# Performance work log

Measured on AMD Instinct MI355X. Metric: run time of the kernel, lower is better.

Reference implementation:

```python
import jax, jax.numpy as jnp
import numpy as np

B, S, D, H, FF = 4, 2048, 1024, 16, 4096
HD = D // H


def setup_inputs() -> dict:
    key = jax.random.key(0)
    ks = jax.random.split(key, 12)
    s = 1.0 / np.sqrt(D)
    sf = 1.0 / np.sqrt(FF)
    return {
        "x": jax.random.normal(ks[0], (B, S, D), dtype=jnp.float32),
        "lengths": jax.random.randint(ks[1], (B,), 1, S + 1, dtype=jnp.int32),
        "qW": jax.random.uniform(ks[2], (D, D), jnp.float32, -s, s),
        "qb": jnp.zeros((D,), jnp.float32),
        "kW": jax.random.uniform(ks[3], (D, D), jnp.float32, -s, s),
        "kb": jnp.zeros((D,), jnp.float32),
        "vW": jax.random.uniform(ks[4], (D, D), jnp.float32, -s, s),
        "vb": jnp.zeros((D,), jnp.float32),
        "oW": jax.random.uniform(ks[5], (D, D), jnp.float32, -s, s),
        "ob": jnp.zeros((D,), jnp.float32),
        "w1": jax.random.uniform(ks[6], (D, FF), jnp.float32, -s, s),
        "b1": jnp.zeros((FF,), jnp.float32),
        "w2": jax.random.uniform(ks[7], (FF, D), jnp.float32, -sf, sf),
        "b2": jnp.zeros((D,), jnp.float32),
    }


def _heads(t):
    # [B,S,D] -> [B,H,S,HD]
    return t.reshape(B, S, H, HD).transpose(0, 2, 1, 3)


def reference(x, lengths, qW, qb, kW, kb, vW, vb, oW, ob, w1, b1, w2, b2):
    q = _heads(x @ qW + qb)
    k = _heads(x @ kW + kb)
    v = _heads(x @ vW + vb)
    scale = 1.0 / np.sqrt(HD)
    logits = jnp.einsum("bhqd,bhkd->bhqk", q, k) * scale  # [B,H,S,S]
    # key-position mask: pos >= length -> -inf
    mask = jnp.arange(S)[None, None, None, :] >= lengths[:, None, None, None]
    logits = jnp.where(mask, -jnp.inf, logits)
    a = jax.nn.softmax(logits, axis=-1)
    ctx = jnp.einsum("bhqk,bhkd->bhqd", a, v)
    ctx = ctx.transpose(0, 2, 1, 3).reshape(B, S, D)
    attn_out = ctx @ oW + ob
    h = jax.nn.relu(attn_out @ w1 + b1)
    return h @ w2 + b2
```

## Files before the change

kernel.cpp:

```cpp
#include <hip/hip_runtime.h>


typedef short bf16x8 __attribute__((ext_vector_type(8)));
typedef float f32x4 __attribute__((ext_vector_type(4)));

__device__ __forceinline__ unsigned short f2bf(float f) {
  unsigned int u = __builtin_bit_cast(unsigned int, f);
  u += 0x7fffu + ((u >> 16) & 1u);
  return (unsigned short)(u >> 16);
}

__device__ __forceinline__ void gload16(const unsigned short* g, unsigned short* l) {
  __builtin_amdgcn_global_load_lds(
      (const __attribute__((address_space(1))) unsigned int*)(g),
      (__attribute__((address_space(3))) unsigned int*)(l),
      16, 0, 0);
}

__global__ __launch_bounds__(256) void cast_f32_bf16(
    const float* __restrict__ src, unsigned short* __restrict__ dst, int n4) {
  int i = blockIdx.x * 256 + threadIdx.x;
  if (i < n4) {
    float4 f = ((const float4*)src)[i];
    ushort4 o;
    o.x = f2bf(f.x); o.y = f2bf(f.y); o.z = f2bf(f.z); o.w = f2bf(f.w);
    ((ushort4*)dst)[i] = o;
  }
}

__global__ __launch_bounds__(256) void prep_weights(
    const float* __restrict__ qW, const float* __restrict__ kW,
    const float* __restrict__ vW, const float* __restrict__ oW,
    const float* __restrict__ w1, const float* __restrict__ w2,
    unsigned short* __restrict__ qWt, unsigned short* __restrict__ kWt,
    unsigned short* __restrict__ vWt, unsigned short* __restrict__ oWt,
    unsigned short* __restrict__ w1t, unsigned short* __restrict__ w2t) {
  const int t = blockIdx.x;
  const float* W; unsigned short* Wt; int N, K, nt, kt;
  if (t < 2048) {
    const int w = t >> 9, r = t & 511;
    nt = r & 15; kt = r >> 4; N = 1024; K = 1024;
    W  = w == 0 ? qW : w == 1 ? kW : w == 2 ? vW : oW;
    Wt = w == 0 ? qWt : w == 1 ? kWt : w == 2 ? vWt : oWt;
  } else if (t < 4096) {
    const int r = t - 2048;
    nt = r & 63; kt = r >> 6; N = 4096; K = 1024; W = w1; Wt = w1t;
  } else {
    const int r = t - 4096;
    nt = r & 15; kt = r >> 4; N = 1024; K = 4096; W = w2; Wt = w2t;
  }
  const int wave = threadIdx.x >> 6, lane = threadIdx.x & 63;
  const int n = nt * 64 + lane;
  const int k0 = kt * 32 + wave * 8;
  union { int4 v; unsigned short u[8]; } s;
#pragma unroll
  for (int j = 0; j < 8; ++j) s.u[j] = f2bf(W[(size_t)(k0 + j) * N + n]);
  *(int4*)(Wt + (size_t)n * K + k0) = s.v;
}

__device__ __forceinline__ void gemm256_core(
    const unsigned short* __restrict__ A, const unsigned short* __restrict__ Bt,
    unsigned short* __restrict__ As, unsigned short* __restrict__ Bs,
    const int m0, const int n0, const int K, f32x4 (&acc)[8][4]) {
  const int tid = (int)threadIdx.x;
  const int w = tid >> 6, l = tid & 63;
  const int quad = l >> 4, l16 = l & 15;
  const int wm = (w >> 2) * 128, wn = (w & 3) * 64;

  const int lr = l >> 2, lc = l & 3;
  const int swz = (lc ^ ((l >> 3) & 3)) * 8;
  const unsigned short* gA[2]; const unsigned short* gB[2];
  unsigned short* dA[2]; unsigned short* dB[2];
#pragma unroll
  for (int j = 0; j < 2; ++j) {
    const int rr = (w * 2 + j) * 16 + lr;
    gA[j] = A + (size_t)(m0 + rr) * K + swz;
    gB[j] = Bt + (size_t)(n0 + rr) * K + swz;
    dA[j] = As + (w * 2 + j) * 512;
    dB[j] = Bs + (w * 2 + j) * 512;
  }

  const int cread = (quad ^ ((l16 >> 1) & 3)) * 8;
  const int rA = (wm + l16) * 32;
  const int rB = (wn + l16) * 32;

  auto STAGE = [&](int db, int t) {
#pragma unroll
    for (int j = 0; j < 2; ++j) {
      gload16(gA[j] + t * 32, dA[j] + db * 8192);
      gload16(gB[j] + t * 32, dB[j] + db * 8192);
    }
  };
  auto COMPUTE = [&](int db) {
    bf16x8 af[8], bf[4];
    const unsigned short* pa = As + db * 8192 + rA + cread;
    const unsigned short* pb = Bs + db * 8192 + rB + cread;
#pragma unroll
    for (int ni = 0; ni < 4; ++ni) bf[ni] = *(const bf16x8*)(pb + ni * 16 * 32);
#pragma unroll
    for (int mi = 0; mi < 8; ++mi) af[mi] = *(const bf16x8*)(pa + mi * 16 * 32);
    __builtin_amdgcn_s_setprio(1);
#pragma unroll
    for (int mi = 0; mi < 8; ++mi)
#pragma unroll
      for (int ni = 0; ni < 4; ++ni)
        acc[mi][ni] = __builtin_amdgcn_mfma_f32_16x16x32_bf16(
            af[mi], bf[ni], acc[mi][ni], 0, 0, 0);
    __builtin_amdgcn_s_setprio(0);
  };

  const int NK = K >> 5;
  STAGE(0, 0); STAGE(1, 1); STAGE(2, 2);
#pragma unroll 1
  for (int t = 0; t < NK - 3; ++t) {
    asm volatile("s_waitcnt vmcnt(8)" ::: "memory");
    __builtin_amdgcn_s_barrier();
    STAGE((t + 3) & 3, t + 3);
    COMPUTE(t & 3);
  }
  asm volatile("s_waitcnt vmcnt(8)" ::: "memory");
  __builtin_amdgcn_s_barrier();
  COMPUTE((NK - 3) & 3);
  asm volatile("s_waitcnt vmcnt(4)" ::: "memory");
  __builtin_amdgcn_s_barrier();
  COMPUTE((NK - 2) & 3);
  asm volatile("s_waitcnt vmcnt(0)" ::: "memory");
  __builtin_amdgcn_s_barrier();
  COMPUTE((NK - 1) & 3);
}

template <int EPI>
__global__ __launch_bounds__(512, 1) void gemm256_bt(
    const unsigned short* __restrict__ A, const unsigned short* __restrict__ Bt,
    const float* __restrict__ bias, void* __restrict__ C, int N, int K) {
  __shared__ unsigned short As[4 * 8192];
  __shared__ unsigned short Bs[4 * 8192];
  const int tn = N >> 8;
  const int cpx = (int)gridDim.x >> 3;
  const int sw = ((int)blockIdx.x & 7) * cpx + ((int)blockIdx.x >> 3);
  const int nt = sw % tn, mt = sw / tn;
  const int m0 = mt * 256, n0 = nt * 256;

  f32x4 acc[8][4] = {};
  gemm256_core(A, Bt, As, Bs, m0, n0, K, acc);

  const int tid = (int)threadIdx.x;
  const int w = tid >> 6, l = tid & 63;
  const int quad = l >> 4, l16 = l & 15;
  const int wm = (w >> 2) * 128, wn = (w & 3) * 64;
#pragma unroll
  for (int ni = 0; ni < 4; ++ni) {
    const int col = n0 + wn + ni * 16 + l16;
    const float bv = bias[col];
#pragma unroll
    for (int mi = 0; mi < 8; ++mi) {
      const int row = m0 + wm + mi * 16 + quad * 4;
#pragma unroll
      for (int r = 0; r < 4; ++r) {
        float v = acc[mi][ni][r] + bv;
        if (EPI == 2) v = v > 0.f ? v : 0.f;
        if (EPI == 0)
          ((float*)C)[(size_t)(row + r) * N + col] = v;
        else
          ((unsigned short*)C)[(size_t)(row + r) * N + col] = f2bf(v);
      }
    }
  }
}

#define QSCALE 0.180336884f

__global__ __launch_bounds__(512, 1) void gemm256_qkv(
    const unsigned short* __restrict__ A, const unsigned short* __restrict__ Bt,
    const float* __restrict__ qb, const float* __restrict__ kb,
    const float* __restrict__ vb, unsigned short* __restrict__ Qo,
    unsigned short* __restrict__ Ko, unsigned short* __restrict__ Vto, int K) {
  __shared__ unsigned short As[4 * 8192];
  __shared__ unsigned short Bs[4 * 8192];
  const int tn = 12;
  const int cpx = (int)gridDim.x >> 3;
  const int sw = ((int)blockIdx.x & 7) * cpx + ((int)blockIdx.x >> 3);
  const int nt = sw % tn, mt = sw / tn;
  const int m0 = mt * 256, n0 = nt * 256;

  f32x4 acc[8][4] = {};
  gemm256_core(A, Bt, As, Bs, m0, n0, K, acc);

  const int tid = (int)threadIdx.x;
  const int w = tid >> 6, l = tid & 63;
  const int quad = l >> 4, l16 = l & 15;
  const int wm = (w >> 2) * 128, wn = (w & 3) * 64;

  const int seg = n0 >> 10;
  const float* bias = seg == 0 ? qb : (seg == 1 ? kb : vb);
#pragma unroll
  for (int ni = 0; ni < 4; ++ni) {
    const int col = (n0 + wn + ni * 16 + l16) & 1023;
    const float bv = bias[col];
#pragma unroll
    for (int mi = 0; mi < 8; ++mi) {
      const int row = m0 + wm + mi * 16 + quad * 4;
      if (seg == 2) {
        const int b = row >> 11, s = row & 2047;
        const int hh = col >> 6, dh = col & 63;
        union { ushort4 v; unsigned short u[4]; } pk;
#pragma unroll
        for (int r = 0; r < 4; ++r) pk.u[r] = f2bf(acc[mi][ni][r] + bv);
        *(ushort4*)(Vto + ((size_t)((b * 16 + hh) * 64 + dh)) * 2048 + s) = pk.v;
      } else if (seg == 0) {
#pragma unroll
        for (int r = 0; r < 4; ++r)
          Qo[(size_t)(row + r) * 1024 + col] = f2bf((acc[mi][ni][r] + bv) * QSCALE);
      } else {
#pragma unroll
        for (int r = 0; r < 4; ++r)
          Ko[(size_t)(row + r) * 1024 + col] = f2bf(acc[mi][ni][r] + bv);
      }
    }
  }
}

template <int EPI>
__global__ __launch_bounds__(256) void gemm_bt(
    const unsigned short* __restrict__ A, const unsigned short* __restrict__ Bt,
    const float* __restrict__ bias, void* __restrict__ C,
    int M, int N, int K) {
  __shared__ unsigned short As[128 * 32];
  __shared__ unsigned short Bs[128 * 32];

  const int tid = threadIdx.x;
  const int wave = tid >> 6, lane = tid & 63;
  const int quad = lane >> 4, l16 = lane & 15;
  const int wm = (wave >> 1) * 64, wn = (wave & 1) * 64;

  const int NT = N >> 7, band = NT >> 3;
  const int xcd = blockIdx.x & 7, local = blockIdx.x >> 3;
  const int nt = xcd * band + local % band;
  const int mt = local / band;
  const int m0 = mt * 128, n0 = nt * 128;

  const int u1 = tid, u2 = 256 + tid;
  const int r1 = u1 >> 2, c1 = (u1 & 3) * 8;
  const int r2 = u2 >> 2, c2 = (u2 & 3) * 8;
  const unsigned short* ga1 = A + (size_t)(m0 + r1) * K + c1;
  const unsigned short* ga2 = A + (size_t)(m0 + r2) * K + c2;
  const unsigned short* gb1 = Bt + (size_t)(n0 + r1) * K + c1;
  const unsigned short* gb2 = Bt + (size_t)(n0 + r2) * K + c2;
  unsigned short* lA1 = As + wave * 512;
  unsigned short* lA2 = As + 2048 + wave * 512;
  unsigned short* lB1 = Bs + wave * 512;
  unsigned short* lB2 = Bs + 2048 + wave * 512;

  f32x4 acc[4][4] = {};

  for (int k0 = 0; k0 < K; k0 += 32) {
    __syncthreads();
    gload16(ga1 + k0, lA1);
    gload16(ga2 + k0, lA2);
    gload16(gb1 + k0, lB1);
    gload16(gb2 + k0, lB2);
    __syncthreads();

    bf16x8 af[4], bfr[4];
#pragma unroll
    for (int mi = 0; mi < 4; ++mi)
      af[mi] = *(const bf16x8*)(As + (wm + mi * 16 + l16) * 32 + quad * 8);
#pragma unroll
    for (int ni = 0; ni < 4; ++ni)
      bfr[ni] = *(const bf16x8*)(Bs + (wn + ni * 16 + l16) * 32 + quad * 8);
#pragma unroll
    for (int mi = 0; mi < 4; ++mi)
#pragma unroll
      for (int ni = 0; ni < 4; ++ni)
        acc[mi][ni] = __builtin_amdgcn_mfma_f32_16x16x32_bf16(
            af[mi], bfr[ni], acc[mi][ni], 0, 0, 0);
  }

#pragma unroll
  for (int ni = 0; ni < 4; ++ni) {
    const int col = n0 + wn + ni * 16 + l16;
    const float bv = bias[col];
#pragma unroll
    for (int mi = 0; mi < 4; ++mi) {
      const int row = m0 + wm + mi * 16 + quad * 4;
#pragma unroll
      for (int r = 0; r < 4; ++r) {
        float v = acc[mi][ni][r] + bv;
        if (EPI == 2) v = v > 0.f ? v : 0.f;
        if (EPI == 0)
          ((float*)C)[(size_t)(row + r) * N + col] = v;
        else
          ((unsigned short*)C)[(size_t)(row + r) * N + col] = f2bf(v);
      }
    }
  }
}

__global__ __launch_bounds__(256, 4) void attn_fused(
    const unsigned short* __restrict__ Q, const unsigned short* __restrict__ K,
    const unsigned short* __restrict__ Vt, const int* __restrict__ lengths,
    unsigned short* __restrict__ ctx) {
  constexpr int S = 2048, D = 1024;
  __shared__ unsigned short Ks[64 * 72];
  __shared__ unsigned short Vs[64 * 72];
  __shared__ unsigned short Ps[4 * 32 * 72];

  const int tid = threadIdx.x;
  const int wave = tid >> 6, lane = tid & 63;
  const int quad = lane >> 4, l16 = lane & 15;
  const int bid = blockIdx.x;
  const int qt = bid & 15;
  const int h = (bid >> 4) & 15;
  const int b = bid >> 8;
  const int q0 = qt * 128;
  const int len = lengths[b];
  const int ktEnd = (len + 63) >> 6;
  const float NEGINF = -__builtin_inff();

  const size_t xbase = (size_t)b * S * D + (size_t)h * 64;
  const size_t vtb = (size_t)(b * 16 + h) * 64;

  bf16x8 qf0[2], qf1[2];
#pragma unroll
  for (int mb = 0; mb < 2; ++mb) {
    const unsigned short* qrow =
        Q + xbase + (size_t)(q0 + wave * 32 + mb * 16 + l16) * D;
    qf0[mb] = *(const bf16x8*)(qrow + quad * 8);
    qf1[mb] = *(const bf16x8*)(qrow + 32 + quad * 8);
  }

  const int sr1 = tid >> 3, sc1 = (tid & 7) * 8;
  const int sr2 = (256 + tid) >> 3, sc2 = (tid & 7) * 8;
  const unsigned short* kg1 = K + xbase + (size_t)sr1 * D + sc1;
  const unsigned short* kg2 = K + xbase + (size_t)sr2 * D + sc2;
  const unsigned short* vg1 = Vt + (vtb + sr1) * S + sc1;
  const unsigned short* vg2 = Vt + (vtb + sr2) * S + sc2;

  f32x4 oacc[2][4] = {};
  float rs[2][4] = {};

  unsigned short* pw = Ps + wave * (32 * 72);

  for (int kt = 0; kt < ktEnd; ++kt) {
    const int k0 = kt * 64;
    __syncthreads();
    *(int4*)(Ks + sr1 * 72 + sc1) = *(const int4*)(kg1 + (size_t)k0 * D);
    *(int4*)(Ks + sr2 * 72 + sc2) = *(const int4*)(kg2 + (size_t)k0 * D);
    *(int4*)(Vs + sr1 * 72 + sc1) = *(const int4*)(vg1 + k0);
    *(int4*)(Vs + sr2 * 72 + sc2) = *(const int4*)(vg2 + k0);
    __syncthreads();

    f32x4 sf[2][4];
#pragma unroll
    for (int cb = 0; cb < 4; ++cb) {
      const bf16x8 kf0 = *(const bf16x8*)(Ks + (cb * 16 + l16) * 72 + quad * 8);
      const bf16x8 kf1 = *(const bf16x8*)(Ks + (cb * 16 + l16) * 72 + 32 + quad * 8);
#pragma unroll
      for (int mb = 0; mb < 2; ++mb) {
        f32x4 c = {0.f, 0.f, 0.f, 0.f};
        c = __builtin_amdgcn_mfma_f32_16x16x32_bf16(qf0[mb], kf0, c, 0, 0, 0);
        c = __builtin_amdgcn_mfma_f32_16x16x32_bf16(qf1[mb], kf1, c, 0, 0, 0);
        sf[mb][cb] = c;
      }
    }

    if (k0 + 64 > len) {
#pragma unroll
      for (int cb = 0; cb < 4; ++cb) {
        const bool msk = (k0 + cb * 16 + l16) >= len;
#pragma unroll
        for (int mb = 0; mb < 2; ++mb)
#pragma unroll
          for (int r = 0; r < 4; ++r) sf[mb][cb][r] = msk ? NEGINF : sf[mb][cb][r];
      }
    }

#pragma unroll
    for (int mb = 0; mb < 2; ++mb)
#pragma unroll
      for (int cb = 0; cb < 4; ++cb)
#pragma unroll
        for (int r = 0; r < 4; ++r) {
          const float p = __builtin_amdgcn_exp2f(sf[mb][cb][r]);
          sf[mb][cb][r] = p;
          rs[mb][r] += p;
        }

#pragma unroll
    for (int mb = 0; mb < 2; ++mb)
#pragma unroll
      for (int cb = 0; cb < 4; ++cb)
#pragma unroll
        for (int r = 0; r < 4; ++r)
          pw[(mb * 16 + quad * 4 + r) * 72 + cb * 16 + l16] = f2bf(sf[mb][cb][r]);

    bf16x8 pa0[2], pa1[2];
#pragma unroll
    for (int mb = 0; mb < 2; ++mb) {
      pa0[mb] = *(const bf16x8*)(pw + (mb * 16 + l16) * 72 + quad * 8);
      pa1[mb] = *(const bf16x8*)(pw + (mb * 16 + l16) * 72 + 32 + quad * 8);
    }
#pragma unroll
    for (int cb = 0; cb < 4; ++cb) {
      const bf16x8 vb0 = *(const bf16x8*)(Vs + (cb * 16 + l16) * 72 + quad * 8);
      const bf16x8 vb1 = *(const bf16x8*)(Vs + (cb * 16 + l16) * 72 + 32 + quad * 8);
#pragma unroll
      for (int mb = 0; mb < 2; ++mb) {
        oacc[mb][cb] = __builtin_amdgcn_mfma_f32_16x16x32_bf16(pa0[mb], vb0, oacc[mb][cb], 0, 0, 0);
        oacc[mb][cb] = __builtin_amdgcn_mfma_f32_16x16x32_bf16(pa1[mb], vb1, oacc[mb][cb], 0, 0, 0);
      }
    }
  }

#pragma unroll
  for (int off = 8; off > 0; off >>= 1)
#pragma unroll
    for (int mb = 0; mb < 2; ++mb)
#pragma unroll
      for (int r = 0; r < 4; ++r) rs[mb][r] += __shfl_xor(rs[mb][r], off, 16);

#pragma unroll
  for (int mb = 0; mb < 2; ++mb) {
    float inv[4];
#pragma unroll
    for (int r = 0; r < 4; ++r) inv[r] = 1.0f / rs[mb][r];
#pragma unroll
    for (int cb = 0; cb < 4; ++cb)
#pragma unroll
      for (int r = 0; r < 4; ++r) {
        const int row = q0 + wave * 32 + mb * 16 + quad * 4 + r;
        ctx[xbase + (size_t)row * D + cb * 16 + l16] = f2bf(oacc[mb][cb][r] * inv[r]);
      }
  }
}

extern "C" void kernel_launch(void* const* d_in, const int* in_sizes, int n_in,
                              void* d_out, int out_size, void* d_ws,
                              size_t ws_size, hipStream_t stream) {
  const float* x  = (const float*)d_in[0];
  const int* lengths = (const int*)d_in[1];
  const float* qW = (const float*)d_in[2];
  const float* qb = (const float*)d_in[3];
  const float* kW = (const float*)d_in[4];
  const float* kb = (const float*)d_in[5];
  const float* vW = (const float*)d_in[6];
  const float* vb = (const float*)d_in[7];
  const float* oW = (const float*)d_in[8];
  const float* ob = (const float*)d_in[9];
  const float* w1 = (const float*)d_in[10];
  const float* b1 = (const float*)d_in[11];
  const float* w2 = (const float*)d_in[12];
  const float* b2 = (const float*)d_in[13];
  float* out = (float*)d_out;

  const int Bx = 4, S = 2048, D = 1024, FF = 4096;
  const int M = Bx * S;

  unsigned short* p = (unsigned short*)d_ws;
  unsigned short* xb  = p; p += (size_t)M * D;
  unsigned short* qWt = p; p += (size_t)D * D;
  unsigned short* kWt = p; p += (size_t)D * D;
  unsigned short* vWt = p; p += (size_t)D * D;
  unsigned short* oWt = p; p += (size_t)D * D;
  unsigned short* w1t = p; p += (size_t)D * FF;
  unsigned short* w2t = p; p += (size_t)FF * D;
  unsigned short* Qb  = p; p += (size_t)M * D;
  unsigned short* Kb  = p; p += (size_t)M * D;
  unsigned short* Vtb = p; p += (size_t)M * D;
  unsigned short* Cb  = p; p += (size_t)M * D;
  unsigned short* Ab  = p; p += (size_t)M * D;
  unsigned short* Hb  = p; p += (size_t)M * FF;

  {
    int n4 = (int)((size_t)M * D / 4);
    cast_f32_bf16<<<dim3((n4 + 255) / 256), dim3(256), 0, stream>>>(x, xb, n4);
  }
  prep_weights<<<dim3(6144), dim3(256), 0, stream>>>(
      qW, kW, vW, oW, w1, w2, qWt, kWt, vWt, oWt, w1t, w2t);

  gemm256_qkv<<<dim3(384), dim3(512), 0, stream>>>(
      xb, qWt, qb, kb, vb, Qb, Kb, Vtb, D);

  attn_fused<<<dim3(Bx * 16 * (S / 128)), dim3(256), 0, stream>>>(
      Qb, Kb, Vtb, lengths, Cb);

  gemm_bt<1><<<dim3((D / 128) * (M / 128)), dim3(256), 0, stream>>>(
      Cb, oWt, ob, Ab, M, D, D);
  gemm256_bt<2><<<dim3(512), dim3(512), 0, stream>>>(Ab, w1t, b1, Hb, FF, D);
  gemm_bt<0><<<dim3((D / 128) * (M / 128)), dim3(256), 0, stream>>>(
      Hb, w2t, b2, out, M, D, FF);
}
```

Measured before the change: 529.0 us.

## Add pipelined 128-tile GEMM core and prefetch K/V tiles in attention

Adds a 128x128 GEMM core with a 4-stage global-to-LDS async pipeline and swizzled LDS layout. The output-projection and FF2 GEMMs switch to it from the single-buffered kernel, and the QKV projection moves from 256 tiles to 128 tiles to get more blocks in flight. The attention kernel now register-prefetches the next K/V tile during compute. The aim is to hide memory latency and improve occupancy and wave balance, at the cost of more LDS and register pressure and smaller tiles for QKV.

```diff
diff --git a/kernel.cpp b/kernel.cpp
--- a/kernel.cpp
+++ b/kernel.cpp
@@ -129,6 +129,77 @@
   COMPUTE((NK - 1) & 3);
 }
 
+__device__ __forceinline__ void gemm128_core(
+    const unsigned short* __restrict__ A, const unsigned short* __restrict__ Bt,
+    unsigned short* __restrict__ As, unsigned short* __restrict__ Bs,
+    const int m0, const int n0, const int K, f32x4 (&acc)[4][4]) {
+  const int tid = (int)threadIdx.x;
+  const int w = tid >> 6, l = tid & 63;
+  const int quad = l >> 4, l16 = l & 15;
+  const int wm = (w >> 1) * 64, wn = (w & 1) * 64;
+
+  const int lr = l >> 2, lc = l & 3;
+  const int swz = (lc ^ ((l >> 3) & 3)) * 8;
+  const unsigned short* gA[2]; const unsigned short* gB[2];
+  unsigned short* dA[2]; unsigned short* dB[2];
+#pragma unroll
+  for (int j = 0; j < 2; ++j) {
+    const int rr = (w * 2 + j) * 16 + lr;
+    gA[j] = A + (size_t)(m0 + rr) * K + swz;
+    gB[j] = Bt + (size_t)(n0 + rr) * K + swz;
+    dA[j] = As + (w * 2 + j) * 512;
+    dB[j] = Bs + (w * 2 + j) * 512;
+  }
+
+  const int cread = (quad ^ ((l16 >> 1) & 3)) * 8;
+  const int rA = (wm + l16) * 32;
+  const int rB = (wn + l16) * 32;
+
+  auto STAGE = [&](int db, int t) {
+#pragma unroll
+    for (int j = 0; j < 2; ++j) {
+      gload16(gA[j] + t * 32, dA[j] + db * 4096);
+      gload16(gB[j] + t * 32, dB[j] + db * 4096);
+    }
+  };
+  auto COMPUTE = [&](int db) {
+    bf16x8 af[4], bf[4];
+    const unsigned short* pa = As + db * 4096 + rA + cread;
+    const unsigned short* pb = Bs + db * 4096 + rB + cread;
+#pragma unroll
+    for (int ni = 0; ni < 4; ++ni) bf[ni] = *(const bf16x8*)(pb + ni * 16 * 32);
+#pragma unroll
+    for (int mi = 0; mi < 4; ++mi) af[mi] = *(const bf16x8*)(pa + mi * 16 * 32);
+    __builtin_amdgcn_s_setprio(1);
+#pragma unroll
+    for (int mi = 0; mi < 4; ++mi)
+#pragma unroll
+      for (int ni = 0; ni < 4; ++ni)
+        acc[mi][ni] = __builtin_amdgcn_mfma_f32_16x16x32_bf16(
+            af[mi], bf[ni], acc[mi][ni], 0, 0, 0);
+    __builtin_amdgcn_s_setprio(0);
+  };
+
+  const int NK = K >> 5;
+  STAGE(0, 0); STAGE(1, 1); STAGE(2, 2);
+#pragma unroll 1
+  for (int t = 0; t < NK - 3; ++t) {
+    asm volatile("s_waitcnt vmcnt(8)" ::: "memory");
+    __builtin_amdgcn_s_barrier();
+    STAGE((t + 3) & 3, t + 3);
+    COMPUTE(t & 3);
+  }
+  asm volatile("s_waitcnt vmcnt(8)" ::: "memory");
+  __builtin_amdgcn_s_barrier();
+  COMPUTE((NK - 3) & 3);
+  asm volatile("s_waitcnt vmcnt(4)" ::: "memory");
+  __builtin_amdgcn_s_barrier();
+  COMPUTE((NK - 2) & 3);
+  asm volatile("s_waitcnt vmcnt(0)" ::: "memory");
+  __builtin_amdgcn_s_barrier();
+  COMPUTE((NK - 1) & 3);
+}
+
 template <int EPI>
 __global__ __launch_bounds__(512, 1) void gemm256_bt(
     const unsigned short* __restrict__ A, const unsigned short* __restrict__ Bt,
@@ -168,114 +239,25 @@
   }
 }
 
-#define QSCALE 0.180336884f
-
-__global__ __launch_bounds__(512, 1) void gemm256_qkv(
+template <int EPI>
+__global__ __launch_bounds__(256, 2) void gemm128_bt(
     const unsigned short* __restrict__ A, const unsigned short* __restrict__ Bt,
-    const float* __restrict__ qb, const float* __restrict__ kb,
-    const float* __restrict__ vb, unsigned short* __restrict__ Qo,
-    unsigned short* __restrict__ Ko, unsigned short* __restrict__ Vto, int K) {
-  __shared__ unsigned short As[4 * 8192];
-  __shared__ unsigned short Bs[4 * 8192];
-  const int tn = 12;
-  const int cpx = (int)gridDim.x >> 3;
-  const int sw = ((int)blockIdx.x & 7) * cpx + ((int)blockIdx.x >> 3);
-  const int nt = sw % tn, mt = sw / tn;
-  const int m0 = mt * 256, n0 = nt * 256;
-
-  f32x4 acc[8][4] = {};
-  gemm256_core(A, Bt, As, Bs, m0, n0, K, acc);
-
-  const int tid = (int)threadIdx.x;
-  const int w = tid >> 6, l = tid & 63;
-  const int quad = l >> 4, l16 = l & 15;
-  const int wm = (w >> 2) * 128, wn = (w & 3) * 64;
-
-  const int seg = n0 >> 10;
-  const float* bias = seg == 0 ? qb : (seg == 1 ? kb : vb);
-#pragma unroll
-  for (int ni = 0; ni < 4; ++ni) {
-    const int col = (n0 + wn + ni * 16 + l16) & 1023;
-    const float bv = bias[col];
-#pragma unroll
-    for (int mi = 0; mi < 8; ++mi) {
-      const int row = m0 + wm + mi * 16 + quad * 4;
-      if (seg == 2) {
-        const int b = row >> 11, s = row & 2047;
-        const int hh = col >> 6, dh = col & 63;
-        union { ushort4 v; unsigned short u[4]; } pk;
-#pragma unroll
-        for (int r = 0; r < 4; ++r) pk.u[r] = f2bf(acc[mi][ni][r] + bv);
-        *(ushort4*)(Vto + ((size_t)((b * 16 + hh) * 64 + dh)) * 2048 + s) = pk.v;
-      } else if (seg == 0) {
-#pragma unroll
-        for (int r = 0; r < 4; ++r)
-          Qo[(size_t)(row + r) * 1024 + col] = f2bf((acc[mi][ni][r] + bv) * QSCALE);
-      } else {
-#pragma unroll
-        for (int r = 0; r < 4; ++r)
-          Ko[(size_t)(row + r) * 1024 + col] = f2bf(acc[mi][ni][r] + bv);
-      }
-    }
-  }
-}
-
-template <int EPI>
-__global__ __launch_bounds__(256) void gemm_bt(
-    const unsigned short* __restrict__ A, const unsigned short* __restrict__ Bt,
-    const float* __restrict__ bias, void* __restrict__ C,
-    int M, int N, int K) {
-  __shared__ unsigned short As[128 * 32];
-  __shared__ unsigned short Bs[128 * 32];
-
-  const int tid = threadIdx.x;
-  const int wave = tid >> 6, lane = tid & 63;
-  const int quad = lane >> 4, l16 = lane & 15;
-  const int wm = (wave >> 1) * 64, wn = (wave & 1) * 64;
-
+    const float* __restrict__ bias, void* __restrict__ C, int N, int K) {
+  __shared__ unsigned short As[4 * 4096];
+  __shared__ unsigned short Bs[4 * 4096];
   const int NT = N >> 7, band = NT >> 3;
   const int xcd = blockIdx.x & 7, local = blockIdx.x >> 3;
   const int nt = xcd * band + local % band;
   const int mt = local / band;
   const int m0 = mt * 128, n0 = nt * 128;
 
-  const int u1 = tid, u2 = 256 + tid;
-  const int r1 = u1 >> 2, c1 = (u1 & 3) * 8;
-  const int r2 = u2 >> 2, c2 = (u2 & 3) * 8;
-  const unsigned short* ga1 = A + (size_t)(m0 + r1) * K + c1;
-  const unsigned short* ga2 = A + (size_t)(m0 + r2) * K + c2;
-  const unsigned short* gb1 = Bt + (size_t)(n0 + r1) * K + c1;
-  const unsigned short* gb2 = Bt + (size_t)(n0 + r2) * K + c2;
-  unsigned short* lA1 = As + wave * 512;
-  unsigned short* lA2 = As + 2048 + wave * 512;
-  unsigned short* lB1 = Bs + wave * 512;
-  unsigned short* lB2 = Bs + 2048 + wave * 512;
-
   f32x4 acc[4][4] = {};
-
-  for (int k0 = 0; k0 < K; k0 += 32) {
-    __syncthreads();
-    gload16(ga1 + k0, lA1);
-    gload16(ga2 + k0, lA2);
-    gload16(gb1 + k0, lB1);
-    gload16(gb2 + k0, lB2);
-    __syncthreads();
-
-    bf16x8 af[4], bfr[4];
-#pragma unroll
-    for (int mi = 0; mi < 4; ++mi)
-      af[mi] = *(const bf16x8*)(As + (wm + mi * 16 + l16) * 32 + quad * 8);
-#pragma unroll
-    for (int ni = 0; ni < 4; ++ni)
-      bfr[ni] = *(const bf16x8*)(Bs + (wn + ni * 16 + l16) * 32 + quad * 8);
-#pragma unroll
-    for (int mi = 0; mi < 4; ++mi)
-#pragma unroll
-      for (int ni = 0; ni < 4; ++ni)
-        acc[mi][ni] = __builtin_amdgcn_mfma_f32_16x16x32_bf16(
-            af[mi], bfr[ni], acc[mi][ni], 0, 0, 0);
-  }
-
+  gemm128_core(A, Bt, As, Bs, m0, n0, K, acc);
+
+  const int tid = (int)threadIdx.x;
+  const int w = tid >> 6, l = tid & 63;
+  const int quad = l >> 4, l16 = l & 15;
+  const int wm = (w >> 1) * 64, wn = (w & 1) * 64;
 #pragma unroll
   for (int ni = 0; ni < 4; ++ni) {
     const int col = n0 + wn + ni * 16 + l16;
@@ -291,6 +273,58 @@
           ((float*)C)[(size_t)(row + r) * N + col] = v;
         else
           ((unsigned short*)C)[(size_t)(row + r) * N + col] = f2bf(v);
+      }
+    }
+  }
+}
+
+#define QSCALE 0.180336884f
+
+__global__ __launch_bounds__(256, 2) void gemm128_qkv(
+    const unsigned short* __restrict__ A, const unsigned short* __restrict__ Bt,
+    const float* __restrict__ qb, const float* __restrict__ kb,
+    const float* __restrict__ vb, unsigned short* __restrict__ Qo,
+    unsigned short* __restrict__ Ko, unsigned short* __restrict__ Vto, int K) {
+  __shared__ unsigned short As[4 * 4096];
+  __shared__ unsigned short Bs[4 * 4096];
+  const int NT = 24, band = 3;
+  const int xcd = blockIdx.x & 7, local = blockIdx.x >> 3;
+  const int nt = xcd * band + local % band;
+  const int mt = local / band;
+  const int m0 = mt * 128, n0 = nt * 128;
+
+  f32x4 acc[4][4] = {};
+  gemm128_core(A, Bt, As, Bs, m0, n0, K, acc);
+
+  const int tid = (int)threadIdx.x;
+  const int w = tid >> 6, l = tid & 63;
+  const int quad = l >> 4, l16 = l & 15;
+  const int wm = (w >> 1) * 64, wn = (w & 1) * 64;
+
+  const int seg = n0 >> 10;
+  const float* bias = seg == 0 ? qb : (seg == 1 ? kb : vb);
+#pragma unroll
+  for (int ni = 0; ni < 4; ++ni) {
+    const int col = (n0 + wn + ni * 16 + l16) & 1023;
+    const float bv = bias[col];
+#pragma unroll
+    for (int mi = 0; mi < 4; ++mi) {
+      const int row = m0 + wm + mi * 16 + quad * 4;
+      if (seg == 2) {
+        const int b = row >> 11, s = row & 2047;
+        const int hh = col >> 6, dh = col & 63;
+        union { ushort4 v; unsigned short u[4]; } pk;
+#pragma unroll
+        for (int r = 0; r < 4; ++r) pk.u[r] = f2bf(acc[mi][ni][r] + bv);
+        *(ushort4*)(Vto + ((size_t)((b * 16 + hh) * 64 + dh)) * 2048 + s) = pk.v;
+      } else if (seg == 0) {
+#pragma unroll
+        for (int r = 0; r < 4; ++r)
+          Qo[(size_t)(row + r) * 1024 + col] = f2bf((acc[mi][ni][r] + bv) * QSCALE);
+      } else {
+#pragma unroll
+        for (int r = 0; r < 4; ++r)
+          Ko[(size_t)(row + r) * 1024 + col] = f2bf(acc[mi][ni][r] + bv);
       }
     }
   }
@@ -341,14 +375,30 @@
 
   unsigned short* pw = Ps + wave * (32 * 72);
 
+  int4 kr1, kr2, vr1, vr2;
+  {
+    kr1 = *(const int4*)(kg1);
+    kr2 = *(const int4*)(kg2);
+    vr1 = *(const int4*)(vg1);
+    vr2 = *(const int4*)(vg2);
+  }
+
   for (int kt = 0; kt < ktEnd; ++kt) {
     const int k0 = kt * 64;
     __syncthreads();
-    *(int4*)(Ks + sr1 * 72 + sc1) = *(const int4*)(kg1 + (size_t)k0 * D);
-    *(int4*)(Ks + sr2 * 72 + sc2) = *(const int4*)(kg2 + (size_t)k0 * D);
-    *(int4*)(Vs + sr1 * 72 + sc1) = *(const int4*)(vg1 + k0);
-    *(int4*)(Vs + sr2 * 72 + sc2) = *(const int4*)(vg2 + k0);
+    *(int4*)(Ks + sr1 * 72 + sc1) = kr1;
+    *(int4*)(Ks + sr2 * 72 + sc2) = kr2;
+    *(int4*)(Vs + sr1 * 72 + sc1) = vr1;
+    *(int4*)(Vs + sr2 * 72 + sc2) = vr2;
     __syncthreads();
+
+    if (kt + 1 < ktEnd) {
+      const int kn = (kt + 1) * 64;
+      kr1 = *(const int4*)(kg1 + (size_t)kn * D);
+      kr2 = *(const int4*)(kg2 + (size_t)kn * D);
+      vr1 = *(const int4*)(vg1 + kn);
+      vr2 = *(const int4*)(vg2 + kn);
+    }
 
     f32x4 sf[2][4];
 #pragma unroll
@@ -478,15 +528,13 @@
   prep_weights<<<dim3(6144), dim3(256), 0, stream>>>(
       qW, kW, vW, oW, w1, w2, qWt, kWt, vWt, oWt, w1t, w2t);
 
-  gemm256_qkv<<<dim3(384), dim3(512), 0, stream>>>(
+  gemm128_qkv<<<dim3(1536), dim3(256), 0, stream>>>(
       xb, qWt, qb, kb, vb, Qb, Kb, Vtb, D);
 
   attn_fused<<<dim3(Bx * 16 * (S / 128)), dim3(256), 0, stream>>>(
       Qb, Kb, Vtb, lengths, Cb);
 
-  gemm_bt<1><<<dim3((D / 128) * (M / 128)), dim3(256), 0, stream>>>(
-      Cb, oWt, ob, Ab, M, D, D);
+  gemm128_bt<1><<<dim3(512), dim3(256), 0, stream>>>(Cb, oWt, ob, Ab, D, D);
   gemm256_bt<2><<<dim3(512), dim3(512), 0, stream>>>(Ab, w1t, b1, Hb, FF, D);
-  gemm_bt<0><<<dim3((D / 128) * (M / 128)), dim3(256), 0, stream>>>(
-      Hb, w2t, b2, out, M, D, FF);
-}
+  gemm128_bt<0><<<dim3(512), dim3(256), 0, stream>>>(Hb, w2t, b2, out, D, FF);
+}
```

Result: faster. 505.2 us (-4.5%).
